# Kernel optimization log

Measured on AMD Instinct MI355X. Metric: run time of the kernel, lower is better.

## Reference

```python
import jax, jax.numpy as jnp
import numpy as np

# Config (matches init_kwargs)
N, A, H, W = 4, 16, 384, 384
B_SIZE = 8      # block_size per spatial dim
STRIDE = 4      # block_stride per spatial dim (overlapping blocks)
THRESH = 2.0    # singular-value soft threshold
NB = (H - B_SIZE) // STRIDE + 1   # blocks per spatial dim (95)
P = B_SIZE * B_SIZE               # pixels per block (64)


def _block_indices():
    """Flat pixel index for each (block, in-block pixel): [NB*NB, P] int32."""
    starts = np.arange(NB) * STRIDE
    ih = starts[:, None] + np.arange(B_SIZE)              # [NB, b] row coords
    flat = ih[:, None, :, None] * W + ih[None, :, None, :]  # [NBh, NBw, b, b]
    return flat.reshape(NB * NB, P).astype(np.int32)


def setup_inputs() -> dict:
    key = jax.random.key(0)
    x = jax.random.normal(key, (N, A, H, W), dtype=jnp.float32)
    idx = jnp.asarray(_block_indices())
    # precompute_normalization: overlap-add of ones -> per-pixel block count
    block_weights = jnp.zeros(H * W, jnp.float32).at[idx].add(1.0).reshape(H, W)
    return {"x": x, "block_weights": block_weights}


def reference(x, block_weights):
    idx = jnp.asarray(_block_indices())           # [B, P]
    # self.shift = (0, 0) on the first forward call -> rolls are identity
    x = jnp.roll(x, (0, 0), axis=(-2, -1))
    xf = x.reshape(N, A, H * W)
    blocks = xf[:, :, idx]                        # [N, A, B, P] block extraction
    m = jnp.transpose(blocks, (0, 2, 3, 1))       # 'n a b p -> n b p a' -> [N,B,P,A]
    U, S, Vh = jnp.linalg.svd(m, full_matrices=False)  # U:[N,B,P,A] S:[N,B,A] Vh:[N,B,A,A]
    S = jnp.maximum(S - THRESH, 0.0)              # soft-threshold singular values
    m = (U * S[..., None, :]) @ Vh                # U diag(S) Vh, [N,B,P,A]
    blocks = jnp.transpose(m, (0, 3, 1, 2))       # 'n b p a -> n a b p'
    # adjoint: overlap-add fold, then normalize by block counts
    out = jnp.zeros((N, A, H * W), x.dtype).at[:, :, idx].add(blocks)
    out = out.reshape(N, A, H, W) / block_weights
    return jnp.roll(out, (0, 0), axis=(-2, -1))
```

## Files before the change

### kernel.cpp

```cpp
#include <hip/hip_runtime.h>


typedef __attribute__((ext_vector_type(2))) float v2f;
typedef union { float4 f4; v2f v2[2]; } f4v2;

#define N_      4
#define A_      16
#define H_      384
#define W_      384
#define PLANE_  (H_*W_)
#define NB_     95
#define NBB_    (NB_*NB_)
#define NMAT_   (N_*NBB_)
#define NWAVE_  ((NMAT_ + 3) / 4)
#define NSWEEP_ 4
#define PHI_BYTES_ ((size_t)NMAT_ * 256 * 4)

__device__ __forceinline__ v2f pk_fma(v2f a, v2f b, v2f c) {
    v2f d; asm("v_pk_fma_f32 %0, %1, %2, %3" : "=v"(d) : "v"(a), "v"(b), "v"(c));
    return d;
}
__device__ __forceinline__ v2f pk_mul(v2f a, v2f b) {
    v2f d; asm("v_pk_mul_f32 %0, %1, %2" : "=v"(d) : "v"(a), "v"(b));
    return d;
}
__device__ __forceinline__ v2f pk_add(v2f a, v2f b) {
    v2f d; asm("v_pk_add_f32 %0, %1, %2" : "=v"(d) : "v"(a), "v"(b));
    return d;
}

template<int CTRL>
__device__ __forceinline__ float dpp16(float v) {
    union { float f; int i; } u; u.f = v;
    u.i = __builtin_amdgcn_mov_dpp(u.i, CTRL, 0xF, 0xF, true);
    return u.f;
}

#define QP1_ 0xB1
#define QP2_ 0x4E
#define QP3_ 0x1B
#define HM_  0x141
#define FM_  0x140
#define R8_  0x128

template<int M>
__device__ __forceinline__ float lane_xor16(float v) {
    if constexpr (M == 1)       return dpp16<QP1_>(v);
    else if constexpr (M == 2)  return dpp16<QP2_>(v);
    else if constexpr (M == 3)  return dpp16<QP3_>(v);
    else if constexpr (M == 7)  return dpp16<HM_>(v);
    else if constexpr (M == 8)  return dpp16<R8_>(v);
    else if constexpr (M == 15) return dpp16<FM_>(v);
    else if constexpr (M == 4)  return dpp16<QP3_>(dpp16<HM_>(v));
    else if constexpr (M == 5)  return dpp16<QP2_>(dpp16<HM_>(v));
    else if constexpr (M == 6)  return dpp16<QP1_>(dpp16<HM_>(v));
    else if constexpr (M == 9)  return dpp16<QP1_>(dpp16<R8_>(v));
    else if constexpr (M == 10) return dpp16<QP2_>(dpp16<R8_>(v));
    else if constexpr (M == 11) return dpp16<QP3_>(dpp16<R8_>(v));
    else if constexpr (M == 12) return dpp16<QP3_>(dpp16<FM_>(v));
    else if constexpr (M == 13) return dpp16<QP2_>(dpp16<FM_>(v));
    else                        return dpp16<QP1_>(dpp16<FM_>(v));
}

template<int M>
__device__ __forceinline__ void jacobi_round(v2f w[8], float& nrm, const int j) {
    v2f pw[8];
    #pragma unroll
    for (int i = 0; i < 8; ++i) {
        pw[i][0] = lane_xor16<M>(w[i][0]);
        pw[i][1] = lane_xor16<M>(w[i][1]);
    }
    const float pn = lane_xor16<M>(nrm);

    v2f d0 = pk_mul(w[0], pw[0]), d1 = pk_mul(w[1], pw[1]);
    #pragma unroll
    for (int i = 2; i < 8; i += 2) {
        d0 = pk_fma(w[i],   pw[i],   d0);
        d1 = pk_fma(w[i+1], pw[i+1], d1);
    }
    const v2f ds = pk_add(d0, d1);
    const float gam = ds[0] + ds[1];

    const bool  low = ((j ^ M) > j);
    const float na  = low ? nrm : pn;
    const float nb  = low ? pn  : nrm;

    const float thr = 1e-12f * (na + nb);
    const bool  rot = fabsf(gam) > thr;
    const float gs  = rot ? gam : 1.f;
    const float zeta = (nb - na) * (0.5f * __builtin_amdgcn_rcpf(gs));
    const float rt   = __builtin_amdgcn_rcpf(
                           fabsf(zeta) +
                           __builtin_amdgcn_sqrtf(__builtin_fmaf(zeta, zeta, 1.f)));
    float t  = copysignf(rt, zeta);
    float c  = __builtin_amdgcn_rsqf(__builtin_fmaf(t, t, 1.f));
    float sv = c * t;
    if (!rot) { c = 1.f; sv = 0.f; t = 0.f; }

    const float ss = low ? -sv : sv;
    const v2f c2 = {c, c}, sp = {ss, ss};
    #pragma unroll
    for (int i = 0; i < 8; ++i)
        w[i] = pk_fma(c2, w[i], pk_mul(sp, pw[i]));

    nrm = __builtin_fmaf(low ? -t : t, gam, nrm);
}

__device__ __forceinline__ void gram_jacobi_phi(
        const float* __restrict__ x, const int wid, const int warp,
        const int lane, float Gl[4][4][320]) {
    const int g   = lane >> 4;
    const int j   = lane & 15;
    const int kq4 = g * 4;
    const int cst = lane & 15;
    const int rh  = lane >> 4;
    float* const mt = &Gl[warp][3][0];

    auto sbase = [&](int s) -> const float* {
        const int id  = wid * 4 + s;
        const int n   = id / NBB_;
        const int rem = id % NBB_;
        const int bi  = rem / NB_;
        const int bj  = rem % NB_;
        return x + n * (A_ * PLANE_) + bi*4*W_ + bj*4
                 + cst * PLANE_ + (rh >> 1) * W_ + (rh & 1) * 4;
    };

    const float* p0 = sbase(0);
    float4 va = *(const float4*)(p0);
    float4 vb = *(const float4*)(p0 + 2*W_);
    float4 vc = *(const float4*)(p0 + 4*W_);
    float4 vd = *(const float4*)(p0 + 6*W_);

    #pragma unroll
    for (int s = 0; s < 4; ++s) {
        float4 na_, nb_, nc_, nd_;
        if (s < 3) {
            const float* pn_ = sbase(s + 1);
            na_ = *(const float4*)(pn_);
            nb_ = *(const float4*)(pn_ + 2*W_);
            nc_ = *(const float4*)(pn_ + 4*W_);
            nd_ = *(const float4*)(pn_ + 6*W_);
        }

        v2f acc0 = {0,0}, acc1 = {0,0}, acc2 = {0,0}, acc3 = {0,0};
        #pragma unroll
        for (int q = 0; q < 4; ++q) {
            __builtin_amdgcn_wave_barrier();
            const float4 vq = (q == 0) ? va : (q == 1) ? vb : (q == 2) ? vc : vd;
            *(float4*)&mt[cst*20 + rh*4] = vq;
            __builtin_amdgcn_wave_barrier();

            #pragma unroll
            for (int p4 = 0; p4 < 16; p4 += 4) {
                f4v2 av, b0, b1, b2, b3;
                av.f4 = *(const float4*)&mt[j*20 + p4];
                b0.f4 = *(const float4*)&mt[(kq4 + 0)*20 + p4];
                b1.f4 = *(const float4*)&mt[(kq4 + 1)*20 + p4];
                b2.f4 = *(const float4*)&mt[(kq4 + 2)*20 + p4];
                b3.f4 = *(const float4*)&mt[(kq4 + 3)*20 + p4];
                #pragma unroll
                for (int h = 0; h < 2; ++h) {
                    acc0 = pk_fma(av.v2[h], b0.v2[h], acc0);
                    acc1 = pk_fma(av.v2[h], b1.v2[h], acc1);
                    acc2 = pk_fma(av.v2[h], b2.v2[h], acc2);
                    acc3 = pk_fma(av.v2[h], b3.v2[h], acc3);
                }
            }
            __builtin_amdgcn_wave_barrier();
        }
        *(float4*)&Gl[warp][s][j*20 + kq4] =
            make_float4(acc0[0]+acc0[1], acc1[0]+acc1[1],
                        acc2[0]+acc2[1], acc3[0]+acc3[1]);
        if (s < 3) { va = na_; vb = nb_; vc = nc_; vd = nd_; }
    }
    __builtin_amdgcn_wave_barrier();

    v2f w[8];
    {
        f4v2 t0, t1, t2, t3;
        t0.f4 = *(const float4*)&Gl[warp][g][j*20 + 0];
        t1.f4 = *(const float4*)&Gl[warp][g][j*20 + 4];
        t2.f4 = *(const float4*)&Gl[warp][g][j*20 + 8];
        t3.f4 = *(const float4*)&Gl[warp][g][j*20 + 12];
        w[0]=t0.v2[0]; w[1]=t0.v2[1]; w[2]=t1.v2[0]; w[3]=t1.v2[1];
        w[4]=t2.v2[0]; w[5]=t2.v2[1]; w[6]=t3.v2[0]; w[7]=t3.v2[1];
    }
    float nrm;
    {
        v2f d = pk_mul(w[0], w[0]);
        #pragma unroll
        for (int i = 1; i < 8; ++i) d = pk_fma(w[i], w[i], d);
        nrm = d[0] + d[1];
    }

    for (int sweep = 0; sweep < NSWEEP_; ++sweep) {
        jacobi_round<1>(w, nrm, j);  jacobi_round<2>(w, nrm, j);
        jacobi_round<3>(w, nrm, j);  jacobi_round<4>(w, nrm, j);
        jacobi_round<5>(w, nrm, j);  jacobi_round<6>(w, nrm, j);
        jacobi_round<7>(w, nrm, j);  jacobi_round<8>(w, nrm, j);
        jacobi_round<9>(w, nrm, j);  jacobi_round<10>(w, nrm, j);
        jacobi_round<11>(w, nrm, j); jacobi_round<12>(w, nrm, j);
        jacobi_round<13>(w, nrm, j); jacobi_round<14>(w, nrm, j);
        jacobi_round<15>(w, nrm, j);
    }
    {
        v2f d = pk_mul(w[0], w[0]);
        #pragma unroll
        for (int i = 1; i < 8; ++i) d = pk_fma(w[i], w[i], d);
        nrm = d[0] + d[1];
    }
    float rho = 0.f;
    if (nrm > 16.f) {
        const float lam = __builtin_amdgcn_sqrtf(nrm);
        rho = (1.f - 2.f * __builtin_amdgcn_rsqf(lam)) * __builtin_amdgcn_rcpf(nrm);
    }

    __builtin_amdgcn_wave_barrier();
    *(float4*)&Gl[warp][g][j*20 + 0]  = make_float4(w[0][0], w[0][1], w[1][0], w[1][1]);
    *(float4*)&Gl[warp][g][j*20 + 4]  = make_float4(w[2][0], w[2][1], w[3][0], w[3][1]);
    *(float4*)&Gl[warp][g][j*20 + 8]  = make_float4(w[4][0], w[4][1], w[5][0], w[5][1]);
    *(float4*)&Gl[warp][g][j*20 + 12] = make_float4(w[6][0], w[6][1], w[7][0], w[7][1]);
    Gl[warp][g][j*20 + 16] = rho;
    __builtin_amdgcn_wave_barrier();

    v2f ph[8];
    #pragma unroll
    for (int i = 0; i < 8; ++i) ph[i] = (v2f){0.f, 0.f};
    #pragma unroll
    for (int k = 0; k < 16; ++k) {
        const float coef = Gl[warp][g][k*20 + 16] * Gl[warp][g][k*20 + j];
        const v2f cf = {coef, coef};
        f4v2 c0, c1, c2r, c3;
        c0.f4  = *(const float4*)&Gl[warp][g][k*20 + 0];
        c1.f4  = *(const float4*)&Gl[warp][g][k*20 + 4];
        c2r.f4 = *(const float4*)&Gl[warp][g][k*20 + 8];
        c3.f4  = *(const float4*)&Gl[warp][g][k*20 + 12];
        ph[0] = pk_fma(cf, c0.v2[0],  ph[0]);
        ph[1] = pk_fma(cf, c0.v2[1],  ph[1]);
        ph[2] = pk_fma(cf, c1.v2[0],  ph[2]);
        ph[3] = pk_fma(cf, c1.v2[1],  ph[3]);
        ph[4] = pk_fma(cf, c2r.v2[0], ph[4]);
        ph[5] = pk_fma(cf, c2r.v2[1], ph[5]);
        ph[6] = pk_fma(cf, c3.v2[0],  ph[6]);
        ph[7] = pk_fma(cf, c3.v2[1],  ph[7]);
    }
    __builtin_amdgcn_wave_barrier();
    *(float4*)&Gl[warp][g][j*20 + 0]  = make_float4(ph[0][0], ph[0][1], ph[1][0], ph[1][1]);
    *(float4*)&Gl[warp][g][j*20 + 4]  = make_float4(ph[2][0], ph[2][1], ph[3][0], ph[3][1]);
    *(float4*)&Gl[warp][g][j*20 + 8]  = make_float4(ph[4][0], ph[4][1], ph[5][0], ph[5][1]);
    *(float4*)&Gl[warp][g][j*20 + 12] = make_float4(ph[6][0], ph[6][1], ph[7][0], ph[7][1]);
    __builtin_amdgcn_wave_barrier();
}

__global__ __launch_bounds__(256, 8)
void llr_phi(const float* __restrict__ x, float* __restrict__ phiG) {
    __shared__ __align__(16) float Gl[4][4][320];
    const int warp = threadIdx.x >> 6;
    const int lane = threadIdx.x & 63;

    const int xcd = blockIdx.x & 7, idx = blockIdx.x >> 3;
    const int wg  = (xcd == 0 ? idx : 283 + (xcd - 1) * 282 + idx);
    const int wid = wg * 4 + warp;
    if (wid >= NWAVE_) return;

    gram_jacobi_phi(x, wid, warp, lane, Gl);

    const int g = lane >> 4, j = lane & 15;
    float* pb = phiG + (size_t)(wid*4 + g) * 256 + j * 16;
    const float4 p0 = *(const float4*)&Gl[warp][g][j*20 + 0];
    const float4 p1 = *(const float4*)&Gl[warp][g][j*20 + 4];
    const float4 p2 = *(const float4*)&Gl[warp][g][j*20 + 8];
    const float4 p3 = *(const float4*)&Gl[warp][g][j*20 + 12];
    *(float4*)&pb[0]  = p0;  *(float4*)&pb[4]  = p1;
    *(float4*)&pb[8]  = p2;  *(float4*)&pb[12] = p3;
}

__global__ __launch_bounds__(256, 8)
void llr_out2(const float* __restrict__ x, const float* __restrict__ phiG,
              float* __restrict__ out) {
    __shared__ __align__(16) float Sl[16][260];

    const int b  = (blockIdx.x & 7) * 288 + (blockIdx.x >> 3);
    const int n  = b / 576;
    const int tt = b % 576;
    const int tr = tt / 12, tc = tt % 12;
    const int r0 = tr*8, c0 = tc*32;
    const int cr0 = tr*2, cc0 = tc*8;

    {
        const int lc = threadIdx.x >> 4;
        const int fo = (threadIdx.x & 15) * 4;
        const int ci = cr0 + (lc >> 3);
        const int cj = cc0 + (lc & 7);
        const int bi0 = max(ci - 1, 0), bi1 = min(ci, NB_ - 1);
        const int bj0 = max(cj - 1, 0), bj1 = min(cj, NB_ - 1);
        const size_t r00 = ((size_t)(n*NBB_ + bi0*NB_ + bj0))*256;
        const size_t r01 = ((size_t)(n*NBB_ + bi0*NB_ + bj1))*256;
        const size_t r10 = ((size_t)(n*NBB_ + bi1*NB_ + bj0))*256;
        const size_t r11 = ((size_t)(n*NBB_ + bi1*NB_ + bj1))*256;
        #pragma unroll
        for (int it = 0; it < 4; ++it) {
            const int off = fo + it*64;
            const float4 a  = *(const float4*)&phiG[r00 + off];
            const float4 bq = *(const float4*)&phiG[r01 + off];
            const float4 cq = *(const float4*)&phiG[r10 + off];
            const float4 d  = *(const float4*)&phiG[r11 + off];
            float4 s;
            s.x = (a.x + bq.x + cq.x + d.x) * 0.25f;
            s.y = (a.y + bq.y + cq.y + d.y) * 0.25f;
            s.z = (a.z + bq.z + cq.z + d.z) * 0.25f;
            s.w = (a.w + bq.w + cq.w + d.w) * 0.25f;
            *(float4*)&Sl[lc][off] = s;
        }
    }
    __syncthreads();

    const int r = threadIdx.x >> 5;
    const int c = threadIdx.x & 31;
    const int lcc = ((r >> 2) << 3) + (c >> 2);
    const size_t sb = (size_t)n * (A_*PLANE_) + (size_t)(r0 + r) * W_ + (c0 + c);

    float xk[16];
    #pragma unroll
    for (int k = 0; k < 16; ++k) xk[k] = x[sb + (size_t)k * PLANE_];

    v2f acc[8];
    #pragma unroll
    for (int i = 0; i < 8; ++i) acc[i] = (v2f){0.f, 0.f};
    #pragma unroll
    for (int k = 0; k < 16; ++k) {
        const v2f xv = {xk[k], xk[k]};
        f4v2 s0, s1, s2, s3;
        s0.f4 = *(const float4*)&Sl[lcc][k*16 + 0];
        s1.f4 = *(const float4*)&Sl[lcc][k*16 + 4];
        s2.f4 = *(const float4*)&Sl[lcc][k*16 + 8];
        s3.f4 = *(const float4*)&Sl[lcc][k*16 + 12];
        acc[0] = pk_fma(xv, s0.v2[0], acc[0]);
        acc[1] = pk_fma(xv, s0.v2[1], acc[1]);
        acc[2] = pk_fma(xv, s1.v2[0], acc[2]);
        acc[3] = pk_fma(xv, s1.v2[1], acc[3]);
        acc[4] = pk_fma(xv, s2.v2[0], acc[4]);
        acc[5] = pk_fma(xv, s2.v2[1], acc[5]);
        acc[6] = pk_fma(xv, s3.v2[0], acc[6]);
        acc[7] = pk_fma(xv, s3.v2[1], acc[7]);
    }
    #pragma unroll
    for (int i = 0; i < 8; ++i) {
        out[sb + (size_t)(2*i)     * PLANE_] = acc[i][0];
        out[sb + (size_t)(2*i + 1) * PLANE_] = acc[i][1];
    }
}

__global__ __launch_bounds__(256, 5)
void llr_fused(const float* __restrict__ x, float* __restrict__ out) {
    __shared__ __align__(16) float Gl[4][4][320];
    const int warp = threadIdx.x >> 6;
    const int lane = threadIdx.x & 63;
    const int wid  = blockIdx.x * 4 + warp;
    if (wid >= NWAVE_) return;

    gram_jacobi_phi(x, wid, warp, lane, Gl);

    const int pr = lane >> 3, pc = lane & 7;
    for (int s = 0; s < 4; ++s) {
        const int id = wid*4 + s;
        const int n = id / NBB_, rem = id % NBB_;
        const int bi = rem / NB_, bj = rem % NB_;
        const int base = n*(A_*PLANE_) + (bi*4+pr)*W_ + (bj*4+pc);
        float mr[16];
        #pragma unroll
        for (int a = 0; a < 16; ++a) mr[a] = x[base + a*PLANE_];
        float o[16];
        #pragma unroll
        for (int a = 0; a < 16; ++a) o[a] = 0.f;
        #pragma unroll
        for (int k = 0; k < 16; ++k) {
            const float mk = mr[k];
            const float4 f0 = *(const float4*)&Gl[warp][s][k*20 + 0];
            const float4 f1 = *(const float4*)&Gl[warp][s][k*20 + 4];
            const float4 f2 = *(const float4*)&Gl[warp][s][k*20 + 8];
            const float4 f3 = *(const float4*)&Gl[warp][s][k*20 + 12];
            o[0]+=mk*f0.x;  o[1]+=mk*f0.y;  o[2]+=mk*f0.z;  o[3]+=mk*f0.w;
            o[4]+=mk*f1.x;  o[5]+=mk*f1.y;  o[6]+=mk*f1.z;  o[7]+=mk*f1.w;
            o[8]+=mk*f2.x;  o[9]+=mk*f2.y;  o[10]+=mk*f2.z; o[11]+=mk*f2.w;
            o[12]+=mk*f3.x; o[13]+=mk*f3.y; o[14]+=mk*f3.z; o[15]+=mk*f3.w;
        }
        #pragma unroll
        for (int a = 0; a < 16; ++a)
            unsafeAtomicAdd(&out[base + a*PLANE_], o[a]);
    }
}

__global__ __launch_bounds__(256)
void llr_div(float* __restrict__ out, const float* __restrict__ bw) {
    const int i = (blockIdx.x * 256 + threadIdx.x) * 4;
    float4 o = *(float4*)&out[i];
    const float4 bv = *(const float4*)&bw[i % PLANE_];
    o.x /= bv.x; o.y /= bv.y; o.z /= bv.z; o.w /= bv.w;
    *(float4*)&out[i] = o;
}

extern "C" void kernel_launch(void* const* d_in, const int* in_sizes, int n_in,
                              void* d_out, int out_size, void* d_ws, size_t ws_size,
                              hipStream_t stream) {
    (void)in_sizes; (void)n_in;
    const float* x  = (const float*)d_in[0];
    const float* bw = (const float*)d_in[1];
    float* out = (float*)d_out;

    if (ws_size >= PHI_BYTES_) {
        float* phiG = (float*)d_ws;
        hipLaunchKernelGGL(llr_phi,  dim3((NWAVE_ + 3) / 4), dim3(256), 0, stream, x, phiG);
        hipLaunchKernelGGL(llr_out2, dim3(4 * 48 * 12),      dim3(256), 0, stream, x, phiG, out);
    } else {
        hipMemsetAsync(out, 0, (size_t)out_size * sizeof(float), stream);
        hipLaunchKernelGGL(llr_fused, dim3((NWAVE_ + 3) / 4), dim3(256), 0, stream, x, out);
        hipLaunchKernelGGL(llr_div, dim3((N_*A_*PLANE_) / (256*4)), dim3(256), 0, stream, out, bw);
    }
}
```

Before: 198.9 us.

## Compute block Gram matrices with split-bf16 MFMA instead of LDS packed FMAs

```diff
diff --git a/kernel.cpp b/kernel.cpp
--- a/kernel.cpp
+++ b/kernel.cpp
@@ -2,6 +2,8 @@
 
 
 typedef __attribute__((ext_vector_type(2))) float v2f;
+typedef __attribute__((ext_vector_type(4))) float f32x4;
+typedef __attribute__((ext_vector_type(8))) short s16x8;
 typedef union { float4 f4; v2f v2[2]; } f4v2;
 
 #define N_      4
@@ -27,6 +29,36 @@
 __device__ __forceinline__ v2f pk_add(v2f a, v2f b) {
     v2f d; asm("v_pk_add_f32 %0, %1, %2" : "=v"(d) : "v"(a), "v"(b));
     return d;
+}
+
+__device__ __forceinline__ unsigned cvtpk_bf16(float a, float b) {
+    unsigned d;
+    asm("v_cvt_pk_bf16_f32 %0, %1, %2" : "=v"(d) : "v"(a), "v"(b));
+    return d;
+}
+__device__ __forceinline__ float asf_(unsigned u) {
+    union { unsigned u; float f; } x; x.u = u; return x.f;
+}
+typedef union { s16x8 s8; unsigned u[4]; } frag8;
+
+__device__ __forceinline__ void split8(const float4 A, const float4 B,
+                                       frag8& hi, frag8& lo) {
+    hi.u[0] = cvtpk_bf16(A.x, A.y);
+    hi.u[1] = cvtpk_bf16(A.z, A.w);
+    hi.u[2] = cvtpk_bf16(B.x, B.y);
+    hi.u[3] = cvtpk_bf16(B.z, B.w);
+    const float l0 = A.x - asf_(hi.u[0] << 16);
+    const float l1 = A.y - asf_(hi.u[0] & 0xFFFF0000u);
+    const float l2 = A.z - asf_(hi.u[1] << 16);
+    const float l3 = A.w - asf_(hi.u[1] & 0xFFFF0000u);
+    const float l4 = B.x - asf_(hi.u[2] << 16);
+    const float l5 = B.y - asf_(hi.u[2] & 0xFFFF0000u);
+    const float l6 = B.z - asf_(hi.u[3] << 16);
+    const float l7 = B.w - asf_(hi.u[3] & 0xFFFF0000u);
+    lo.u[0] = cvtpk_bf16(l0, l1);
+    lo.u[1] = cvtpk_bf16(l2, l3);
+    lo.u[2] = cvtpk_bf16(l4, l5);
+    lo.u[3] = cvtpk_bf16(l6, l7);
 }
 
 template<int CTRL>
@@ -112,67 +144,35 @@
     const int g   = lane >> 4;
     const int j   = lane & 15;
     const int kq4 = g * 4;
-    const int cst = lane & 15;
-    const int rh  = lane >> 4;
-    float* const mt = &Gl[warp][3][0];
-
-    auto sbase = [&](int s) -> const float* {
+
+    #pragma unroll
+    for (int s = 0; s < 4; ++s) {
         const int id  = wid * 4 + s;
         const int n   = id / NBB_;
         const int rem = id % NBB_;
         const int bi  = rem / NB_;
         const int bj  = rem % NB_;
-        return x + n * (A_ * PLANE_) + bi*4*W_ + bj*4
-                 + cst * PLANE_ + (rh >> 1) * W_ + (rh & 1) * 4;
-    };
-
-    const float* p0 = sbase(0);
-    float4 va = *(const float4*)(p0);
-    float4 vb = *(const float4*)(p0 + 2*W_);
-    float4 vc = *(const float4*)(p0 + 4*W_);
-    float4 vd = *(const float4*)(p0 + 6*W_);
-
-    #pragma unroll
-    for (int s = 0; s < 4; ++s) {
-        float4 na_, nb_, nc_, nd_;
-        if (s < 3) {
-            const float* pn_ = sbase(s + 1);
-            na_ = *(const float4*)(pn_);
-            nb_ = *(const float4*)(pn_ + 2*W_);
-            nc_ = *(const float4*)(pn_ + 4*W_);
-            nd_ = *(const float4*)(pn_ + 6*W_);
-        }
-
-        v2f acc0 = {0,0}, acc1 = {0,0}, acc2 = {0,0}, acc3 = {0,0};
-        #pragma unroll
-        for (int q = 0; q < 4; ++q) {
-            __builtin_amdgcn_wave_barrier();
-            const float4 vq = (q == 0) ? va : (q == 1) ? vb : (q == 2) ? vc : vd;
-            *(float4*)&mt[cst*20 + rh*4] = vq;
-            __builtin_amdgcn_wave_barrier();
-
-            #pragma unroll
-            for (int p4 = 0; p4 < 16; p4 += 4) {
-                f4v2 av, b0, b1, b2, b3;
-                av.f4 = *(const float4*)&mt[j*20 + p4];
-                b0.f4 = *(const float4*)&mt[(kq4 + 0)*20 + p4];
-                b1.f4 = *(const float4*)&mt[(kq4 + 1)*20 + p4];
-                b2.f4 = *(const float4*)&mt[(kq4 + 2)*20 + p4];
-                b3.f4 = *(const float4*)&mt[(kq4 + 3)*20 + p4];
-                #pragma unroll
-                for (int h = 0; h < 2; ++h) {
-                    acc0 = pk_fma(av.v2[h], b0.v2[h], acc0);
-                    acc1 = pk_fma(av.v2[h], b1.v2[h], acc1);
-                    acc2 = pk_fma(av.v2[h], b2.v2[h], acc2);
-                    acc3 = pk_fma(av.v2[h], b3.v2[h], acc3);
-                }
-            }
-            __builtin_amdgcn_wave_barrier();
-        }
-        *(float4*)&Gl[warp][s][j*20 + kq4] =
-            make_float4(acc0[0]+acc0[1], acc1[0]+acc1[1],
-                        acc2[0]+acc2[1], acc3[0]+acc3[1]);
-        if (s < 3) { va = na_; vb = nb_; vc = nc_; vd = nd_; }
+        const float* bp = x + (size_t)n * (A_ * PLANE_) + (size_t)j * PLANE_
+                            + (bi*4 + g) * W_ + bj*4;
+
+        const float4 va = *(const float4*)(bp);
+        const float4 vb = *(const float4*)(bp + 4);
+        const float4 vc = *(const float4*)(bp + 4*W_);
+        const float4 vd = *(const float4*)(bp + 4*W_ + 4);
+
+        frag8 hi0, lo0, hi1, lo1;
+        split8(va, vb, hi0, lo0);
+        split8(vc, vd, hi1, lo1);
+
+        f32x4 C = {0.f, 0.f, 0.f, 0.f};
+        C = __builtin_amdgcn_mfma_f32_16x16x32_bf16(lo0.s8, hi0.s8, C, 0, 0, 0);
+        C = __builtin_amdgcn_mfma_f32_16x16x32_bf16(hi0.s8, lo0.s8, C, 0, 0, 0);
+        C = __builtin_amdgcn_mfma_f32_16x16x32_bf16(hi0.s8, hi0.s8, C, 0, 0, 0);
+        C = __builtin_amdgcn_mfma_f32_16x16x32_bf16(lo1.s8, hi1.s8, C, 0, 0, 0);
+        C = __builtin_amdgcn_mfma_f32_16x16x32_bf16(hi1.s8, lo1.s8, C, 0, 0, 0);
+        C = __builtin_amdgcn_mfma_f32_16x16x32_bf16(hi1.s8, hi1.s8, C, 0, 0, 0);
+
+        *(float4*)&Gl[warp][s][j*20 + kq4] = make_float4(C[0], C[1], C[2], C[3]);
     }
     __builtin_amdgcn_wave_barrier();
 
```

Result: faster. 187.7 us (median of 2 runs) (-5.7%).
